# Kernel tuning notes

Measured on AMD Instinct MI355X. Metric: run time of the kernel, lower is better.

## Reference

```python
import jax, jax.numpy as jnp
import numpy as np

C = 1  # channels (depthwise conv group count)
N_ITER = 10
EPS = 1e-12


def _dwconv(x, w):
    # depthwise valid conv, NCHW input, OIHW weight with O=C, I=1
    return jax.lax.conv_general_dilated(
        x, w, window_strides=(1, 1), padding='VALID',
        dimension_numbers=('NCHW', 'OIHW', 'NCHW'), feature_group_count=C)


def _forward_grad(u, f_grad, f_grad2):
    gx = _dwconv(jnp.pad(u, ((0, 0), (0, 0), (0, 0), (0, 1))), f_grad)
    gx = gx.at[:, :, :, -1].set(0.0)
    gy = _dwconv(jnp.pad(u, ((0, 0), (0, 0), (0, 1), (0, 0))), f_grad2)
    gy = gy.at[:, :, -1, :].set(0.0)
    return gx, gy


def _divergence(px, py, div_w, div_w2):
    tx = jnp.pad(px[:, :, :, :-1], ((0, 0), (0, 0), (0, 0), (1, 0)))
    ty = jnp.pad(py[:, :, :-1, :], ((0, 0), (0, 0), (1, 0), (0, 0)))
    gx = _dwconv(jnp.pad(tx, ((0, 0), (0, 0), (0, 0), (0, 1))), div_w)
    gy = _dwconv(jnp.pad(ty, ((0, 0), (0, 0), (0, 1), (0, 0))), div_w2)
    return gx + gy


def setup_inputs() -> dict:
    key = jax.random.key(0)
    k1, k2 = jax.random.split(key)
    B, H, W = 64, 256, 256
    x = jax.random.normal(k1, (B, C, H, W), dtype=jnp.float32)
    y = jax.random.normal(k2, (B, C, H, W), dtype=jnp.float32)
    img_grad = jnp.tile(jnp.array([[[[-0.5, 0.0, 0.5]]]], jnp.float32), (C, 1, 1, 1))   # (C,1,1,3)
    img_grad2 = jnp.tile(jnp.array([[[[-0.5], [0.0], [0.5]]]], jnp.float32), (C, 1, 1, 1))  # (C,1,3,1)
    f_grad = jnp.tile(jnp.array([[[[-1.0, 1.0]]]], jnp.float32), (C, 1, 1, 1))          # (C,1,1,2)
    f_grad2 = jnp.tile(jnp.array([[[[-1.0], [1.0]]]], jnp.float32), (C, 1, 1, 1))       # (C,1,2,1)
    div_w = jnp.tile(jnp.array([[[[-1.0, 1.0]]]], jnp.float32), (C, 1, 1, 1))
    div_w2 = jnp.tile(jnp.array([[[[-1.0], [1.0]]]], jnp.float32), (C, 1, 1, 1))
    t = jnp.array([0.3], jnp.float32)
    l = jnp.array([0.15], jnp.float32)
    a = jnp.array([0.25], jnp.float32)
    return {'x': x, 'y': y, 'img_grad': img_grad, 'img_grad2': img_grad2,
            'f_grad': f_grad, 'f_grad2': f_grad2, 'div_w': div_w, 'div_w2': div_w2,
            't': t, 'l': l, 'a': a}


def reference(x, y, img_grad, img_grad2, f_grad, f_grad2, div_w, div_w2, t, l, a):
    l_t = (l * t)[0]
    taut = (a / t)[0]
    ts = t[0]

    # centered image gradients of y with replicated boundary corrections from x
    g2x = _dwconv(jnp.pad(y, ((0, 0), (0, 0), (0, 0), (1, 1))), img_grad)
    g2x = g2x.at[:, :, :, 0].set(0.5 * (x[:, :, :, 1] - x[:, :, :, 0]))
    g2x = g2x.at[:, :, :, -1].set(0.5 * (x[:, :, :, -1] - x[:, :, :, -2]))
    g2y = _dwconv(jnp.pad(y, ((0, 0), (0, 0), (1, 1), (0, 0))), img_grad2)
    g2y = g2y.at[:, :, 0, :].set(0.5 * (x[:, :, 1, :] - x[:, :, 0, :]))
    g2y = g2y.at[:, :, -1, :].set(0.5 * (x[:, :, -1, :] - x[:, :, -2, :]))

    grad = g2x * g2x + g2y * g2y + EPS
    u1 = jnp.zeros_like(x)
    u2 = jnp.zeros_like(x)
    rho_c = y - g2x * u1 - g2y * u2 - x  # u1=u2=0 initially
    p11 = jnp.zeros_like(x); p12 = jnp.zeros_like(x)
    p21 = jnp.zeros_like(x); p22 = jnp.zeros_like(x)

    zero = jnp.zeros_like(x)
    for _ in range(N_ITER):
        rho = rho_c + g2x * u1 + g2y * u2 + EPS
        mask1 = rho < -l_t * grad
        mask2 = rho > l_t * grad
        mask3 = (~mask1) & (~mask2) & (grad > EPS)
        s = -rho / grad
        v1 = jnp.where(mask1, l_t * g2x, jnp.where(mask2, -l_t * g2x, jnp.where(mask3, s * g2x, zero)))
        v2 = jnp.where(mask1, l_t * g2y, jnp.where(mask2, -l_t * g2y, jnp.where(mask3, s * g2y, zero)))
        v1 = v1 + u1
        v2 = v2 + u2
        u1 = v1 + ts * _divergence(p11, p12, div_w, div_w2)
        u2 = v2 + ts * _divergence(p21, p22, div_w, div_w2)
        u1x, u1y = _forward_grad(u1, f_grad, f_grad2)
        u2x, u2y = _forward_grad(u2, f_grad, f_grad2)
        n1 = jnp.sqrt(u1x * u1x + u1y * u1y + EPS)
        n2 = jnp.sqrt(u2x * u2x + u2y * u2y + EPS)
        p11 = (p11 + taut * u1x) / (1.0 + taut * n1)
        p12 = (p12 + taut * u1y) / (1.0 + taut * n1)
        p21 = (p21 + taut * u2x) / (1.0 + taut * n2)
        p22 = (p22 + taut * u2y) / (1.0 + taut * n2)
    return (u1, u2)
```

## Files before the change

### kernel.cpp

```cpp
#include <hip/hip_runtime.h>
#include <hip/hip_fp16.h>

#define HH 256
#define WW 256
#define NB 64
#define NPIX (NB * HH * WW)
#define NF4  (NPIX / 4)
#define ROW4 (WW / 4)
#define EPSF 1e-12f
#define NTHR 256
#define NBLK (NF4 / NTHR)
#define FTRH 8
#define FTHR 512
#define TPI  (HH / FTRH)
#define FBLK (NB * TPI)
#define NIT  3
#define NU   (FTRH + 2 * NIT)
#define NPR  (FTRH + 2 * NIT - 1)

__device__ __forceinline__ float4 ld4(const float* p, int f) {
    return ((const float4*)p)[f];
}
__device__ __forceinline__ void st4(float* p, int f, const float* v) {
    ((float4*)p)[f] = make_float4(v[0], v[1], v[2], v[3]);
}
__device__ __forceinline__ void ld8h(const __half2* p, int f, float* a, float* b) {
    float4 raw = ((const float4*)p)[f];
    const __half2* h = (const __half2*)&raw;
    #pragma unroll
    for (int k = 0; k < 4; ++k) {
        float2 v = __half22float2(h[k]);
        a[k] = v.x; b[k] = v.y;
    }
}
__device__ __forceinline__ void st8h(__half2* p, int f, const float* a, const float* b) {
    float4 raw;
    __half2* h = (__half2*)&raw;
    #pragma unroll
    for (int k = 0; k < 4; ++k) h[k] = __floats2half2_rn(a[k], b[k]);
    ((float4*)p)[f] = raw;
}
__device__ __forceinline__ float4 pack4h2(const float* a, const float* b) {
    float4 raw;
    __half2* h = (__half2*)&raw;
    #pragma unroll
    for (int k = 0; k < 4; ++k) h[k] = __floats2half2_rn(a[k], b[k]);
    return raw;
}
__device__ __forceinline__ void unpack4h2(float4 raw, float* a, float* b) {
    const __half2* h = (const __half2*)&raw;
    #pragma unroll
    for (int k = 0; k < 4; ++k) {
        float2 v = __half22float2(h[k]);
        a[k] = v.x; b[k] = v.y;
    }
}
__device__ __forceinline__ void h2w(unsigned int w, float& a, float& b) {
    __half2 h = *(__half2*)&w;
    float2 v = __half22float2(h);
    a = v.x; b = v.y;
}

__device__ __forceinline__ void thresh(
    float gx, float gy, float rho, float grad, float l_t,
    float& v1, float& v2)
{
    float s = -rho * __builtin_amdgcn_rcpf(grad);
    float c = __builtin_amdgcn_fmed3f(s, -l_t, l_t);
    v1 = c * gx; v2 = c * gy;
}

__device__ __forceinline__ void pupd(
    float pao, float pbo, float ux, float uy, float taut,
    float& pa, float& pb)
{
    float n2 = fmaf(ux, ux, fmaf(uy, uy, EPSF));
    float n  = __builtin_amdgcn_sqrtf(n2);
    float r  = __builtin_amdgcn_rcpf(fmaf(taut, n, 1.f));
    pa = fmaf(taut, ux, pao) * r;
    pb = fmaf(taut, uy, pbo) * r;
}

__global__ __launch_bounds__(NTHR) void s_kernel(
    const float* __restrict__ x, const float* __restrict__ y,
    __half2* __restrict__ ga, float* __restrict__ rc)
{
    int f = blockIdx.x * NTHR + threadIdx.x;
    int idx = f << 2;
    int i  = (idx >> 8) & 255;

    float4 xc4 = ld4(x, f), yc4 = ld4(y, f);
    const float* xc = (const float*)&xc4;
    const float* yc = (const float*)&yc4;

    float4 a4, b4;
    if (i == 0)            { a4 = ld4(x, f + ROW4); b4 = xc4; }
    else if (i == HH - 1)  { a4 = xc4; b4 = ld4(x, f - ROW4); }
    else                   { a4 = ld4(y, f + ROW4); b4 = ld4(y, f - ROW4); }
    const float* aa = (const float*)&a4;
    const float* bb = (const float*)&b4;

    float yl = __shfl_up(yc4.w, 1);
    float yr = __shfl_down(yc4.x, 1);

    int j0 = idx & 255;
    float gxo[4], gyo[4], rco[4];
    #pragma unroll
    for (int k = 0; k < 4; ++k) {
        int j = j0 + k;
        float gx;
        if (j == 0)            gx = 0.5f * (xc[1] - xc[0]);
        else if (j == WW - 1)  gx = 0.5f * (xc[3] - xc[2]);
        else {
            float ynext = (k < 3) ? yc[k + 1] : yr;
            float yprev = (k > 0) ? yc[k - 1] : yl;
            gx = 0.5f * (ynext - yprev);
        }
        float gy = 0.5f * (aa[k] - bb[k]);
        gxo[k] = gx; gyo[k] = gy;
        rco[k] = yc[k] - xc[k];
    }
    st8h(ga, f, gxo, gyo); st4(rc, f, rco);
}

template <bool P0, bool LAST>
__global__ __launch_bounds__(FTHR, 8) void fp_kernel(
    const __half2* __restrict__ ga, const float* __restrict__ rc,
    const __half2* __restrict__ upi,
    const __half2* __restrict__ pai, const __half2* __restrict__ pbi,
    __half2* __restrict__ upo,
    float* __restrict__ u1f, float* __restrict__ u2f,
    __half2* __restrict__ pao, __half2* __restrict__ pbo,
    const float* __restrict__ tp, const float* __restrict__ lp,
    const float* __restrict__ ap)
{
    __shared__ alignas(16) __half2 sU [NU ][WW];
    __shared__ alignas(16) __half2 sPA[NPR][WW];
    __shared__ alignas(16) __half2 sPB[NPR][WW];

    const float ts   = tp[0];
    const float l_t  = lp[0] * ts;
    const float taut = ap[0] / ts;

    const int t     = threadIdx.x;
    const int tile  = blockIdx.x;
    const int i0    = (tile & (TPI - 1)) * FTRH;
    const int base4 = (tile / TPI) * (HH * ROW4);

    const int tr  = t >> 6;
    const int tcg = t & 63;
    const int tc  = tcg * 4;

    for (int rr = tr - NIT; rr <= FTRH + NIT - 1; rr += FTRH) {
        int gr = i0 + rr;
        float4* dst = (float4*)&sU[rr + NIT][tc];
        if (gr >= 0 && gr < HH) {
            int f = base4 + gr * ROW4 + tcg;
            if (P0) {
                float gx[4], gy[4];
                ld8h(ga, f, gx, gy);
                float4 rc4 = ld4(rc, f);
                const float* rcv = (const float*)&rc4;
                float v1[4], v2[4];
                #pragma unroll
                for (int k = 0; k < 4; ++k) {
                    float grad = fmaf(gx[k], gx[k], fmaf(gy[k], gy[k], EPSF));
                    float rho  = rcv[k] + EPSF;
                    thresh(gx[k], gy[k], rho, grad, l_t, v1[k], v2[k]);
                }
                *dst = pack4h2(v1, v2);
            } else {
                *dst = ((const float4*)upi)[f];
            }
        } else {
            *dst = make_float4(0.f, 0.f, 0.f, 0.f);
        }
    }
    __syncthreads();

    #pragma unroll
    for (int m = 0; m < NIT; ++m) {
        const int plo = -(NIT - m);
        const int phi = FTRH - 1 + (NIT - 1 - m);
        for (int rr = tr + plo; rr <= phi; rr += FTRH) {
            int gr = i0 + rr;
            int li = rr + NIT;
            if (gr >= 0 && gr < HH) {
                float4 rawU = *(const float4*)&sU[li][tc];
                float u1c[4], u2c[4];
                unpack4h2(rawU, u1c, u2c);
                float u1d[4] = {0,0,0,0}, u2d[4] = {0,0,0,0};
                bool hasDn = (gr < HH - 1);
                if (hasDn) unpack4h2(*(const float4*)&sU[li + 1][tc], u1d, u2d);
                unsigned int w0 = ((const unsigned int*)&rawU)[0];
                unsigned int nb = __shfl_down((int)w0, 1);
                float u1r, u2r;  h2w(nb, u1r, u2r);
                float c11[4], c12[4], c21[4], c22[4];
                if (m == 0) {
                    if (P0) {
                        #pragma unroll
                        for (int k = 0; k < 4; ++k) { c11[k]=c12[k]=c21[k]=c22[k]=0.f; }
                    } else {
                        int f = base4 + gr * ROW4 + tcg;
                        ld8h(pai, f, c11, c12);
                        ld8h(pbi, f, c21, c22);
                    }
                } else {
                    unpack4h2(*(const float4*)&sPA[li][tc], c11, c21);
                    unpack4h2(*(const float4*)&sPB[li][tc], c12, c22);
                }
                float p11n[4], p12n[4], p21n[4], p22n[4];
                #pragma unroll
                for (int k = 0; k < 4; ++k) {
                    int j = tc + k;
                    float du1 = (k < 3) ? u1c[k + 1] : u1r;
                    float du2 = (k < 3) ? u2c[k + 1] : u2r;
                    float u1x = (j < WW - 1) ? du1 - u1c[k] : 0.f;
                    float u2x = (j < WW - 1) ? du2 - u2c[k] : 0.f;
                    float u1y = hasDn ? u1d[k] - u1c[k] : 0.f;
                    float u2y = hasDn ? u2d[k] - u2c[k] : 0.f;
                    pupd(c11[k], c12[k], u1x, u1y, taut, p11n[k], p12n[k]);
                    pupd(c21[k], c22[k], u2x, u2y, taut, p21n[k], p22n[k]);
                }
                *(float4*)&sPA[li][tc] = pack4h2(p11n, p21n);
                *(float4*)&sPB[li][tc] = pack4h2(p12n, p22n);
                if (m == NIT - 1 && !LAST && rr >= 0 && rr < FTRH) {
                    int f = base4 + gr * ROW4 + tcg;
                    st8h(pao, f, p11n, p12n);
                    st8h(pbo, f, p21n, p22n);
                }
            } else {
                *(float4*)&sPA[li][tc] = make_float4(0.f, 0.f, 0.f, 0.f);
                *(float4*)&sPB[li][tc] = make_float4(0.f, 0.f, 0.f, 0.f);
            }
        }
        __syncthreads();

        const int ulo = -(NIT - 1 - m);
        const int uhi = FTRH - 1 + (NIT - 1 - m);
        for (int rr = tr + ulo; rr <= uhi; rr += FTRH) {
            int gr = i0 + rr;
            int li = rr + NIT;
            if (gr < 0 || gr >= HH) continue;
            int f = base4 + gr * ROW4 + tcg;
            float gx[4], gy[4];
            ld8h(ga, f, gx, gy);
            float4 rc4 = ld4(rc, f);
            const float* rcv = (const float*)&rc4;
            float u1c[4], u2c[4];
            unpack4h2(*(const float4*)&sU[li][tc], u1c, u2c);
            float4 rawA = *(const float4*)&sPA[li][tc];
            float p11[4], p21[4], p12[4], p22[4], q12[4], q22[4];
            unpack4h2(rawA, p11, p21);
            unpack4h2(*(const float4*)&sPB[li][tc], p12, p22);
            unpack4h2(*(const float4*)&sPB[li - 1][tc], q12, q22);
            unsigned int w3 = ((const unsigned int*)&rawA)[3];
            unsigned int lw = __shfl_up((int)w3, 1);
            float l11, l21;  h2w(lw, l11, l21);
            if (tcg == 0) { l11 = 0.f; l21 = 0.f; }
            bool hasDn = (gr < HH - 1);
            float u1n[4], u2n[4];
            #pragma unroll
            for (int k = 0; k < 4; ++k) {
                int j = tc + k;
                float t11  = (j < WW - 1) ? p11[k] : 0.f;
                float t21  = (j < WW - 1) ? p21[k] : 0.f;
                float l11k = (k == 0) ? l11 : p11[k - 1];
                float l21k = (k == 0) ? l21 : p21[k - 1];
                float t12  = hasDn ? p12[k] : 0.f;
                float t22  = hasDn ? p22[k] : 0.f;
                float div1 = (t11 - l11k) + (t12 - q12[k]);
                float div2 = (t21 - l21k) + (t22 - q22[k]);

                float grad = fmaf(gx[k], gx[k], fmaf(gy[k], gy[k], EPSF));
                float rho  = rcv[k] + gx[k]*u1c[k] + gy[k]*u2c[k] + EPSF;
                float v1, v2;
                thresh(gx[k], gy[k], rho, grad, l_t, v1, v2);
                u1n[k] = v1 + u1c[k] + ts * div1;
                u2n[k] = v2 + u2c[k] + ts * div2;
            }
            if (m == NIT - 1) {
                if (LAST) { st4(u1f, f, u1n); st4(u2f, f, u2n); }
                else      { st8h(upo, f, u1n, u2n); }
            } else {
                *(float4*)&sU[li][tc] = pack4h2(u1n, u2n);
            }
        }
        if (m < NIT - 1) __syncthreads();
    }
}

extern "C" void kernel_launch(void* const* d_in, const int* in_sizes, int n_in,
                              void* d_out, int out_size, void* d_ws, size_t ws_size,
                              hipStream_t stream) {
    const float* x = (const float*)d_in[0];
    const float* y = (const float*)d_in[1];
    const float* t = (const float*)d_in[8];
    const float* l = (const float*)d_in[9];
    const float* a = (const float*)d_in[10];

    float* u1out = (float*)d_out;
    float* u2out = u1out + NPIX;

    char* ws = (char*)d_ws;
    float*   rcp_ = (float*)ws;                              ws += (size_t)NPIX * 4;
    __half2* gaP  = (__half2*)ws;                            ws += (size_t)NPIX * 4;
    __half2* upA  = (__half2*)ws;                            ws += (size_t)NPIX * 4;
    __half2* upB  = (__half2*)ws;                            ws += (size_t)NPIX * 4;
    __half2* paA  = (__half2*)ws;                            ws += (size_t)NPIX * 4;
    __half2* pbA  = (__half2*)ws;                            ws += (size_t)NPIX * 4;
    __half2* paB  = (__half2*)ws;                            ws += (size_t)NPIX * 4;
    __half2* pbB  = (__half2*)ws;

    s_kernel<<<dim3(NBLK), dim3(NTHR), 0, stream>>>(x, y, gaP, rcp_);

    fp_kernel<true, false><<<dim3(FBLK), dim3(FTHR), 0, stream>>>(
        gaP, rcp_, nullptr, nullptr, nullptr,
        upA, nullptr, nullptr, paA, pbA, t, l, a);

    fp_kernel<false, false><<<dim3(FBLK), dim3(FTHR), 0, stream>>>(
        gaP, rcp_, upA, paA, pbA,
        upB, nullptr, nullptr, paB, pbB, t, l, a);

    fp_kernel<false, true><<<dim3(FBLK), dim3(FTHR), 0, stream>>>(
        gaP, rcp_, upB, paB, pbB,
        nullptr, u1out, u2out, nullptr, nullptr, t, l, a);
}
```

Before: 226.8 us.

## Keep u and p state in registers across fused iterations, drop sPA buffer

```diff
diff --git a/kernel.cpp b/kernel.cpp
--- a/kernel.cpp
+++ b/kernel.cpp
@@ -55,11 +55,6 @@
         a[k] = v.x; b[k] = v.y;
     }
 }
-__device__ __forceinline__ void h2w(unsigned int w, float& a, float& b) {
-    __half2 h = *(__half2*)&w;
-    float2 v = __half22float2(h);
-    a = v.x; b = v.y;
-}
 
 __device__ __forceinline__ void thresh(
     float gx, float gy, float rho, float grad, float l_t,
@@ -124,7 +119,7 @@
 }
 
 template <bool P0, bool LAST>
-__global__ __launch_bounds__(FTHR, 8) void fp_kernel(
+__global__ __launch_bounds__(FTHR, 6) void fp_kernel(
     const __half2* __restrict__ ga, const float* __restrict__ rc,
     const __half2* __restrict__ upi,
     const __half2* __restrict__ pai, const __half2* __restrict__ pbi,
@@ -135,7 +130,6 @@
     const float* __restrict__ ap)
 {
     __shared__ alignas(16) __half2 sU [NU ][WW];
-    __shared__ alignas(16) __half2 sPA[NPR][WW];
     __shared__ alignas(16) __half2 sPB[NPR][WW];
 
     const float ts   = tp[0];
@@ -151,30 +145,46 @@
     const int tcg = t & 63;
     const int tc  = tcg * 4;
 
-    for (int rr = tr - NIT; rr <= FTRH + NIT - 1; rr += FTRH) {
-        int gr = i0 + rr;
-        float4* dst = (float4*)&sU[rr + NIT][tc];
+    float u1[2][4], u2[2][4];
+    float p11[2][4], p12[2][4], p21[2][4], p22[2][4];
+
+    #pragma unroll
+    for (int s = 0; s < 2; ++s) {
+        const int rr = tr - NIT + 8 * s;
+        const int gr = i0 + rr;
+        const int li = rr + NIT;
         if (gr >= 0 && gr < HH) {
-            int f = base4 + gr * ROW4 + tcg;
+            const int f = base4 + gr * ROW4 + tcg;
             if (P0) {
                 float gx[4], gy[4];
                 ld8h(ga, f, gx, gy);
                 float4 rc4 = ld4(rc, f);
                 const float* rcv = (const float*)&rc4;
-                float v1[4], v2[4];
                 #pragma unroll
                 for (int k = 0; k < 4; ++k) {
                     float grad = fmaf(gx[k], gx[k], fmaf(gy[k], gy[k], EPSF));
-                    float rho  = rcv[k] + EPSF;
-                    thresh(gx[k], gy[k], rho, grad, l_t, v1[k], v2[k]);
+                    thresh(gx[k], gy[k], rcv[k] + EPSF, grad, l_t,
+                           u1[s][k], u2[s][k]);
                 }
-                *dst = pack4h2(v1, v2);
             } else {
-                *dst = ((const float4*)upi)[f];
+                ld8h(upi, f, u1[s], u2[s]);
+            }
+            if (!P0 && rr <= FTRH + 1) {
+                ld8h(pai, f, p11[s], p12[s]);
+                ld8h(pbi, f, p21[s], p22[s]);
+            } else {
+                #pragma unroll
+                for (int k = 0; k < 4; ++k)
+                    { p11[s][k]=p12[s][k]=p21[s][k]=p22[s][k]=0.f; }
             }
         } else {
-            *dst = make_float4(0.f, 0.f, 0.f, 0.f);
+            #pragma unroll
+            for (int k = 0; k < 4; ++k) {
+                u1[s][k]=u2[s][k]=0.f;
+                p11[s][k]=p12[s][k]=p21[s][k]=p22[s][k]=0.f;
+            }
         }
+        if (li < NU) *(float4*)&sU[li][tc] = pack4h2(u1[s], u2[s]);
     }
     __syncthreads();
 
@@ -182,108 +192,88 @@
     for (int m = 0; m < NIT; ++m) {
         const int plo = -(NIT - m);
         const int phi = FTRH - 1 + (NIT - 1 - m);
-        for (int rr = tr + plo; rr <= phi; rr += FTRH) {
-            int gr = i0 + rr;
-            int li = rr + NIT;
+
+        #pragma unroll
+        for (int s = 0; s < 2; ++s) {
+            const int rr = tr - NIT + 8 * s;
+            if (rr < plo || rr > phi) continue;
+            const int gr = i0 + rr;
+            const int li = rr + NIT;
             if (gr >= 0 && gr < HH) {
-                float4 rawU = *(const float4*)&sU[li][tc];
-                float u1c[4], u2c[4];
-                unpack4h2(rawU, u1c, u2c);
+                const bool hasDn = (gr < HH - 1);
                 float u1d[4] = {0,0,0,0}, u2d[4] = {0,0,0,0};
-                bool hasDn = (gr < HH - 1);
                 if (hasDn) unpack4h2(*(const float4*)&sU[li + 1][tc], u1d, u2d);
-                unsigned int w0 = ((const unsigned int*)&rawU)[0];
-                unsigned int nb = __shfl_down((int)w0, 1);
-                float u1r, u2r;  h2w(nb, u1r, u2r);
-                float c11[4], c12[4], c21[4], c22[4];
-                if (m == 0) {
-                    if (P0) {
-                        #pragma unroll
-                        for (int k = 0; k < 4; ++k) { c11[k]=c12[k]=c21[k]=c22[k]=0.f; }
-                    } else {
-                        int f = base4 + gr * ROW4 + tcg;
-                        ld8h(pai, f, c11, c12);
-                        ld8h(pbi, f, c21, c22);
-                    }
-                } else {
-                    unpack4h2(*(const float4*)&sPA[li][tc], c11, c21);
-                    unpack4h2(*(const float4*)&sPB[li][tc], c12, c22);
-                }
-                float p11n[4], p12n[4], p21n[4], p22n[4];
+                const float u1r = __shfl_down(u1[s][0], 1);
+                const float u2r = __shfl_down(u2[s][0], 1);
                 #pragma unroll
                 for (int k = 0; k < 4; ++k) {
-                    int j = tc + k;
-                    float du1 = (k < 3) ? u1c[k + 1] : u1r;
-                    float du2 = (k < 3) ? u2c[k + 1] : u2r;
-                    float u1x = (j < WW - 1) ? du1 - u1c[k] : 0.f;
-                    float u2x = (j < WW - 1) ? du2 - u2c[k] : 0.f;
-                    float u1y = hasDn ? u1d[k] - u1c[k] : 0.f;
-                    float u2y = hasDn ? u2d[k] - u2c[k] : 0.f;
-                    pupd(c11[k], c12[k], u1x, u1y, taut, p11n[k], p12n[k]);
-                    pupd(c21[k], c22[k], u2x, u2y, taut, p21n[k], p22n[k]);
+                    const int j = tc + k;
+                    float du1 = (k < 3) ? u1[s][k + 1] : u1r;
+                    float du2 = (k < 3) ? u2[s][k + 1] : u2r;
+                    float u1x = (j < WW - 1) ? du1 - u1[s][k] : 0.f;
+                    float u2x = (j < WW - 1) ? du2 - u2[s][k] : 0.f;
+                    float u1y = hasDn ? u1d[k] - u1[s][k] : 0.f;
+                    float u2y = hasDn ? u2d[k] - u2[s][k] : 0.f;
+                    pupd(p11[s][k], p12[s][k], u1x, u1y, taut,
+                         p11[s][k], p12[s][k]);
+                    pupd(p21[s][k], p22[s][k], u2x, u2y, taut,
+                         p21[s][k], p22[s][k]);
                 }
-                *(float4*)&sPA[li][tc] = pack4h2(p11n, p21n);
-                *(float4*)&sPB[li][tc] = pack4h2(p12n, p22n);
+                *(float4*)&sPB[li][tc] = pack4h2(p12[s], p22[s]);
                 if (m == NIT - 1 && !LAST && rr >= 0 && rr < FTRH) {
-                    int f = base4 + gr * ROW4 + tcg;
-                    st8h(pao, f, p11n, p12n);
-                    st8h(pbo, f, p21n, p22n);
+                    const int f = base4 + gr * ROW4 + tcg;
+                    st8h(pao, f, p11[s], p12[s]);
+                    st8h(pbo, f, p21[s], p22[s]);
                 }
             } else {
-                *(float4*)&sPA[li][tc] = make_float4(0.f, 0.f, 0.f, 0.f);
                 *(float4*)&sPB[li][tc] = make_float4(0.f, 0.f, 0.f, 0.f);
             }
         }
         __syncthreads();
 
-        const int ulo = -(NIT - 1 - m);
-        const int uhi = FTRH - 1 + (NIT - 1 - m);
-        for (int rr = tr + ulo; rr <= uhi; rr += FTRH) {
-            int gr = i0 + rr;
-            int li = rr + NIT;
+        const int ulo = plo + 1, uhi = phi;
+        #pragma unroll
+        for (int s = 0; s < 2; ++s) {
+            const int rr = tr - NIT + 8 * s;
+            if (rr < ulo || rr > uhi) continue;
+            const int gr = i0 + rr;
             if (gr < 0 || gr >= HH) continue;
-            int f = base4 + gr * ROW4 + tcg;
+            const int li = rr + NIT;
+            const int f  = base4 + gr * ROW4 + tcg;
             float gx[4], gy[4];
             ld8h(ga, f, gx, gy);
             float4 rc4 = ld4(rc, f);
             const float* rcv = (const float*)&rc4;
-            float u1c[4], u2c[4];
-            unpack4h2(*(const float4*)&sU[li][tc], u1c, u2c);
-            float4 rawA = *(const float4*)&sPA[li][tc];
-            float p11[4], p21[4], p12[4], p22[4], q12[4], q22[4];
-            unpack4h2(rawA, p11, p21);
-            unpack4h2(*(const float4*)&sPB[li][tc], p12, p22);
+            float q12[4], q22[4];
             unpack4h2(*(const float4*)&sPB[li - 1][tc], q12, q22);
-            unsigned int w3 = ((const unsigned int*)&rawA)[3];
-            unsigned int lw = __shfl_up((int)w3, 1);
-            float l11, l21;  h2w(lw, l11, l21);
+            float l11 = __shfl_up(p11[s][3], 1);
+            float l21 = __shfl_up(p21[s][3], 1);
             if (tcg == 0) { l11 = 0.f; l21 = 0.f; }
-            bool hasDn = (gr < HH - 1);
-            float u1n[4], u2n[4];
+            const bool hasDn = (gr < HH - 1);
             #pragma unroll
             for (int k = 0; k < 4; ++k) {
-                int j = tc + k;
-                float t11  = (j < WW - 1) ? p11[k] : 0.f;
-                float t21  = (j < WW - 1) ? p21[k] : 0.f;
-                float l11k = (k == 0) ? l11 : p11[k - 1];
-                float l21k = (k == 0) ? l21 : p21[k - 1];
-                float t12  = hasDn ? p12[k] : 0.f;
-                float t22  = hasDn ? p22[k] : 0.f;
+                const int j = tc + k;
+                float t11  = (j < WW - 1) ? p11[s][k] : 0.f;
+                float t21  = (j < WW - 1) ? p21[s][k] : 0.f;
+                float l11k = (k == 0) ? l11 : p11[s][k - 1];
+                float l21k = (k == 0) ? l21 : p21[s][k - 1];
+                float t12  = hasDn ? p12[s][k] : 0.f;
+                float t22  = hasDn ? p22[s][k] : 0.f;
                 float div1 = (t11 - l11k) + (t12 - q12[k]);
                 float div2 = (t21 - l21k) + (t22 - q22[k]);
 
                 float grad = fmaf(gx[k], gx[k], fmaf(gy[k], gy[k], EPSF));
-                float rho  = rcv[k] + gx[k]*u1c[k] + gy[k]*u2c[k] + EPSF;
+                float rho  = rcv[k] + gx[k]*u1[s][k] + gy[k]*u2[s][k] + EPSF;
                 float v1, v2;
                 thresh(gx[k], gy[k], rho, grad, l_t, v1, v2);
-                u1n[k] = v1 + u1c[k] + ts * div1;
-                u2n[k] = v2 + u2c[k] + ts * div2;
+                u1[s][k] = v1 + u1[s][k] + ts * div1;
+                u2[s][k] = v2 + u2[s][k] + ts * div2;
             }
             if (m == NIT - 1) {
-                if (LAST) { st4(u1f, f, u1n); st4(u2f, f, u2n); }
-                else      { st8h(upo, f, u1n, u2n); }
+                if (LAST) { st4(u1f, f, u1[s]); st4(u2f, f, u2[s]); }
+                else      { st8h(upo, f, u1[s], u2[s]); }
             } else {
-                *(float4*)&sU[li][tc] = pack4h2(u1n, u2n);
+                *(float4*)&sU[li][tc] = pack4h2(u1[s], u2[s]);
             }
         }
         if (m < NIT - 1) __syncthreads();
```

Measured after the change: 275.3 us. 21.4% more time.
